# Performance work log

Hardware: AMD Instinct MI355X
Metric: run time of the kernel (lower is better)

The kernel has to match this reference:

```python
import jax, jax.numpy as jnp
import numpy as np

C = 256
HEADS = 4
RADIUS = 2
LN_EPS = 1e-5


def setup_inputs() -> dict:
    key = jax.random.key(0)
    ks = jax.random.split(key, 8)
    s = 0.02
    return {
        "feat": jax.random.normal(ks[0], (8, C, 64, 64), dtype=jnp.float32),
        "in_w": jax.random.normal(ks[1], (3 * C, C), dtype=jnp.float32) * s,
        "in_b": jnp.zeros((3 * C,), dtype=jnp.float32),
        "out_w": jax.random.normal(ks[2], (C, C), dtype=jnp.float32) * s,
        "out_b": jnp.zeros((C,), dtype=jnp.float32),
        "proj_w": jax.random.normal(ks[3], (C, 4 * C), dtype=jnp.float32) * s,
        "proj_b": jnp.zeros((C,), dtype=jnp.float32),
        "ln_g": jnp.ones((C,), dtype=jnp.float32),
        "ln_b": jnp.zeros((C,), dtype=jnp.float32),
    }


def _spatial_mask(h, w, radius):
    yy, xx = jnp.meshgrid(jnp.arange(h), jnp.arange(w), indexing="ij")
    coords = jnp.stack([yy.ravel(), xx.ravel()], axis=-1).astype(jnp.float32)  # [N,2]
    dist = jnp.abs(coords[:, None, :] - coords[None, :, :]).sum(-1)  # Manhattan [N,N]
    return jnp.where(dist > radius, -jnp.inf, 0.0).astype(jnp.float32)


def _attend(qf, mf, mask, in_w, in_b, out_w, out_b, proj_w, proj_b, ln_g, ln_b):
    b, c, h, w = qf.shape
    n = h * w
    d = c // HEADS
    qt = qf.reshape(b, c, n).transpose(0, 2, 1)  # [B,N,C]
    mt = mf.reshape(b, c, n).transpose(0, 2, 1)
    q = qt @ in_w[:c].T + in_b[:c]
    k = mt @ in_w[c:2 * c].T + in_b[c:2 * c]
    v = mt @ in_w[2 * c:].T + in_b[2 * c:]
    # [B,H,N,D]
    q = q.reshape(b, n, HEADS, d).transpose(0, 2, 1, 3)
    k = k.reshape(b, n, HEADS, d).transpose(0, 2, 1, 3)
    v = v.reshape(b, n, HEADS, d).transpose(0, 2, 1, 3)
    scores = jnp.einsum("bhnd,bhmd->bhnm", q, k) / jnp.sqrt(jnp.float32(d)) + mask
    attn = jax.nn.softmax(scores, axis=-1)
    ctx = jnp.einsum("bhnm,bhmd->bhnd", attn, v)
    ctx = ctx.transpose(0, 2, 1, 3).reshape(b, n, c) @ out_w.T + out_b  # [B,N,C]
    asym = jnp.concatenate([qt, ctx, jnp.abs(qt - ctx), qt * ctx], axis=-1)
    y = asym @ proj_w.T + proj_b
    mu = y.mean(-1, keepdims=True)
    var = ((y - mu) ** 2).mean(-1, keepdims=True)
    y = (y - mu) / jnp.sqrt(var + LN_EPS) * ln_g + ln_b
    y = jax.nn.relu(y)
    return y.transpose(0, 2, 1).reshape(b, c, h, w)


def reference(feat, in_w, in_b, out_w, out_b, proj_w, proj_b, ln_g, ln_b):
    b, c, h, w = feat.shape
    mid = w // 2
    left = feat[:, :, :, :mid]
    right = feat[:, :, :, mid:]
    right_mirror = right[:, :, :, ::-1]
    left_mirror = left[:, :, :, ::-1]
    mask = _spatial_mask(h, mid, RADIUS)
    args = (mask, in_w, in_b, out_w, out_b, proj_w, proj_b, ln_g, ln_b)
    left_asym = _attend(left, right_mirror, *args)
    right_asym = _attend(right, left_mirror, *args)
    return jnp.concatenate([left_asym, right_asym], axis=-1)
```

## Files before the change

### kernel.cpp

```cpp
#include <hip/hip_runtime.h>
#include <hip/hip_bf16.h>


#define NTOK 32768

using bf16x8 = __attribute__((ext_vector_type(8))) short;
using f32x4  = __attribute__((ext_vector_type(4))) float;

__device__ __forceinline__ float b2f(short s) {
    unsigned u = ((unsigned)(unsigned short)s) << 16;
    union { unsigned u; float f; } c; c.u = u; return c.f;
}
__device__ __forceinline__ short f2b(float f) {
    __hip_bfloat16 h = __float2bfloat16(f);
    return *(short*)&h;
}
__device__ __forceinline__ void async_copy16(const void* g, void* l) {
    __builtin_amdgcn_global_load_lds(
        (const __attribute__((address_space(1))) unsigned int*)g,
        (__attribute__((address_space(3))) unsigned int*)l, 16, 0, 0);
}

__global__ __launch_bounds__(256) void prep_kernel(const float* __restrict__ feat,
                                                   const float* __restrict__ in_w,
                                                   const float* __restrict__ out_w,
                                                   const float* __restrict__ proj_w,
                                                   __hip_bfloat16* __restrict__ X,
                                                   __hip_bfloat16* __restrict__ wbf) {
    const int bid = blockIdx.x;
    const int tid = threadIdx.x;
    if (bid < 4096) {
        __shared__ float tile[32][68];
        const int b   = bid >> 9;
        const int rem = bid & 511;
        const int sp0 = (rem & 63) * 64;
        const int c0  = (rem >> 6) * 32;
        #pragma unroll
        for (int u = 0; u < 2; ++u) {
            const int idx = tid + u * 256;
            const int cl = idx >> 4;
            const int sq = (idx & 15) * 4;
            const float4 v = *(const float4*)(feat + ((size_t)(b * 256 + c0 + cl) << 12) + sp0 + sq);
            tile[cl][sq]     = v.x;
            tile[cl][sq + 1] = v.y;
            tile[cl][sq + 2] = v.z;
            tile[cl][sq + 3] = v.w;
        }
        __syncthreads();
        #pragma unroll
        for (int u = 0; u < 2; ++u) {
            const int idx = tid + u * 256;
            const int tok = idx >> 3;
            const int cq  = (idx & 7) * 4;
            short4 s;
            s.x = f2b(tile[cq][tok]);
            s.y = f2b(tile[cq + 1][tok]);
            s.z = f2b(tile[cq + 2][tok]);
            s.w = f2b(tile[cq + 3][tok]);
            *(short4*)(X + (size_t)(b * 4096 + sp0 + tok) * 256 + c0 + cq) = s;
        }
    } else {
        const int i4 = (bid - 4096) * 1024 + tid * 4;
        if (i4 < 196608) {
            const float4 v = *(const float4*)(in_w + i4);
            short4 s = {f2b(v.x), f2b(v.y), f2b(v.z), f2b(v.w)};
            *(short4*)(wbf + i4) = s;
        }
        if (i4 < 65536) {
            const float4 v = *(const float4*)(out_w + i4);
            short4 s = {f2b(v.x), f2b(v.y), f2b(v.z), f2b(v.w)};
            *(short4*)(wbf + 196608 + i4) = s;
        }
        if (i4 < 262144) {
            const float4 v = *(const float4*)(proj_w + i4);
            short4 s = {f2b(v.x), f2b(v.y), f2b(v.z), f2b(v.w)};
            *(short4*)(wbf + 262144 + i4) = s;
        }
    }
}

template <int KDIM, bool OUT_BF16>
__global__ __launch_bounds__(256) void mfma_gemm(const __hip_bfloat16* __restrict__ A,
                                                 const __hip_bfloat16* __restrict__ W,
                                                 const float* __restrict__ bias,
                                                 void* __restrict__ C, int Ntot) {
    __shared__ __align__(16) short As[128 * 64];
    __shared__ __align__(16) short Bs[128 * 64];
    const int tid = threadIdx.x;
    const int m0 = blockIdx.x * 128;
    const int n0 = blockIdx.y * 128;
    const int wave = tid >> 6, lane = tid & 63;
    const int wm = (wave >> 1) * 64;
    const int wn = (wave & 1) * 64;
    const int fm = lane & 15;
    const int fq = lane >> 4;

    f32x4 acc[4][4] = {};

    for (int k0 = 0; k0 < KDIM; k0 += 64) {
        #pragma unroll
        for (int v = 0; v < 4; ++v) {
            const int qb = v * 256 + wave * 64;
            const int q = qb + lane;
            const int r = q >> 3;
            const int cs = (q & 7) ^ (r & 7);
            async_copy16(A + (size_t)(m0 + r) * KDIM + k0 + cs * 8, &As[qb * 8]);
            async_copy16(W + (size_t)(n0 + r) * KDIM + k0 + cs * 8, &Bs[qb * 8]);
        }
        __syncthreads();
        #pragma unroll
        for (int kk = 0; kk < 2; ++kk) {
            bf16x8 af[4], bw[4];
            #pragma unroll
            for (int i = 0; i < 4; ++i) {
                const int row = wm + i * 16 + fm;
                af[i] = *(const bf16x8*)(&As[row * 64 + (((fq + kk * 4) ^ (fm & 7)) * 8)]);
            }
            #pragma unroll
            for (int j = 0; j < 4; ++j) {
                const int row = wn + j * 16 + fm;
                bw[j] = *(const bf16x8*)(&Bs[row * 64 + (((fq + kk * 4) ^ (fm & 7)) * 8)]);
            }
            #pragma unroll
            for (int i = 0; i < 4; ++i)
                #pragma unroll
                for (int j = 0; j < 4; ++j)
                    acc[i][j] = __builtin_amdgcn_mfma_f32_16x16x32_bf16(af[i], bw[j], acc[i][j], 0, 0, 0);
        }
        __syncthreads();
    }
    #pragma unroll
    for (int j = 0; j < 4; ++j) {
        const int col = n0 + wn + j * 16 + fm;
        const float bv = bias[col];
        #pragma unroll
        for (int i = 0; i < 4; ++i) {
            #pragma unroll
            for (int r = 0; r < 4; ++r) {
                const int row = m0 + wm + i * 16 + fq * 4 + r;
                const float v = acc[i][j][r] + bv;
                if (OUT_BF16)
                    ((__hip_bfloat16*)C)[(size_t)row * Ntot + col] = __float2bfloat16(v);
                else
                    ((float*)C)[(size_t)row * Ntot + col] = v;
            }
        }
    }
}

#define P0DY ((2u)|(2u<<3)|(2u<<6)|(2u<<9)|(2u<<12)|(1u<<15)|(1u<<18)|(1u<<21))
#define P0DX ((2u)|(1u<<3)|(3u<<6)|(0u<<9)|(4u<<12)|(2u<<15)|(1u<<18)|(3u<<21))
#define P1DY ((3u)|(3u<<3)|(3u<<6)|(0u<<9)|(4u<<12)|(2u<<15)|(2u<<18)|(2u<<21))
#define P1DX ((2u)|(1u<<3)|(3u<<6)|(2u<<9)|(2u<<12)|(2u<<15)|(2u<<18)|(2u<<21))

__global__ __launch_bounds__(256) void attn_kernel(const __hip_bfloat16* __restrict__ qkv,
                                                   __hip_bfloat16* __restrict__ ctx) {
    const int t = blockIdx.x * 4 + (threadIdx.x >> 6);
    const int lane = threadIdx.x & 63;
    const int n  = lane >> 3;
    const int cg = lane & 7;
    const int x6 = t & 63;
    const int yq = (t >> 6) & 63;
    const int b  = t >> 12;
    const int side = x6 >> 5;
    const int x = x6 & 31;

    bool valid[2];
    size_t kb[2];
    #pragma unroll
    for (int p = 0; p < 2; ++p) {
        const unsigned dyp = p ? P1DY : P0DY;
        const unsigned dxp = p ? P1DX : P0DX;
        const int sh = 3 * n;
        const int dy = (int)((dyp >> sh) & 7) - 2;
        const int dx = (int)((dxp >> sh) & 7) - 2;
        const int yy = yq + dy, xx = x + dx;
        valid[p] = (p == 0 || n < 5) && yy >= 0 && yy < 64 && xx >= 0 && xx < 32;
        const int xm = side ? (31 - xx) : (63 - xx);
        int tm = (b << 12) + (yy << 6) + xm;
        if (!valid[p]) tm = t;
        kb[p] = (size_t)tm * 768 + 256 + cg * 8;
    }
    const size_t qb = (size_t)t * 768 + cg * 8;
    const size_t ob = (size_t)t * 256;

    #pragma unroll
    for (int hp = 0; hp < 2; ++hp) {
        bf16x8 q8[2], k8[2][2], v8[2][2];
        #pragma unroll
        for (int hh = 0; hh < 2; ++hh) {
            const int h = hp * 2 + hh;
            q8[hh] = *(const bf16x8*)(qkv + qb + h * 64);
            #pragma unroll
            for (int p = 0; p < 2; ++p) {
                k8[hh][p] = *(const bf16x8*)(qkv + kb[p] + h * 64);
                v8[hh][p] = *(const bf16x8*)(qkv + kb[p] + h * 64 + 256);
            }
        }
        #pragma unroll
        for (int hh = 0; hh < 2; ++hh) {
            float sc[2];
            #pragma unroll
            for (int p = 0; p < 2; ++p) {
                float s = 0.f;
                #pragma unroll
                for (int j = 0; j < 8; ++j) s += b2f(q8[hh][j]) * b2f(k8[hh][p][j]);
                s += __shfl_xor(s, 1, 64);
                s += __shfl_xor(s, 2, 64);
                s += __shfl_xor(s, 4, 64);
                sc[p] = valid[p] ? s * 0.125f : -1e30f;
            }
            const float p0 = __expf(sc[0]);
            const float p1 = __expf(sc[1]);
            float l = p0 + p1;
            l += __shfl_xor(l, 8, 64);
            l += __shfl_xor(l, 16, 64);
            l += __shfl_xor(l, 32, 64);

            float o[8];
            #pragma unroll
            for (int j = 0; j < 8; ++j)
                o[j] = p0 * b2f(v8[hh][0][j]) + p1 * b2f(v8[hh][1][j]);
            float r4[4];
            #pragma unroll
            for (int i = 0; i < 4; ++i) {
                const float a = o[2 * i], bb = o[2 * i + 1];
                const float mine = (n & 1) ? bb : a;
                const float theirs = (n & 1) ? a : bb;
                r4[i] = mine + __shfl_xor(theirs, 8, 64);
            }
            float r2[2];
            #pragma unroll
            for (int i = 0; i < 2; ++i) {
                const float a = r4[2 * i], bb = r4[2 * i + 1];
                const float mine = (n & 2) ? bb : a;
                const float theirs = (n & 2) ? a : bb;
                r2[i] = mine + __shfl_xor(theirs, 16, 64);
            }
            float ov;
            {
                const float a = r2[0], bb = r2[1];
                const float mine = (n & 4) ? bb : a;
                const float theirs = (n & 4) ? a : bb;
                ov = mine + __shfl_xor(theirs, 32, 64);
            }
            const float rl = __builtin_amdgcn_rcpf(l);
            ctx[ob + (hp * 2 + hh) * 64 + cg * 8 + n] = __float2bfloat16(ov * rl);
        }
    }
}

__global__ __launch_bounds__(512, 4) void proj_ln_fused(const __hip_bfloat16* __restrict__ X,
                                                        const __hip_bfloat16* __restrict__ CTX,
                                                        const __hip_bfloat16* __restrict__ W2,
                                                        const float* __restrict__ out_b,
                                                        const __hip_bfloat16* __restrict__ W,
                                                        const float* __restrict__ bias,
                                                        const float* __restrict__ ln_g,
                                                        const float* __restrict__ ln_b,
                                                        float* __restrict__ out) {
    __shared__ __align__(16) short smem[36864];
    __shared__ float mu_s[64], inv_s[64];
    short* c2s = smem;
    short* As  = smem + 16384;
    short* Bs  = smem + 20480;
    const int tid = threadIdx.x;
    const int m0 = blockIdx.x * 64;
    const int b = m0 >> 12, sp0 = m0 & 4095;
    const int wave = tid >> 6, lane = tid & 63;
    const int wmh = (wave >> 2) * 32;
    const int wn  = (wave & 3) * 64;
    const int fm = lane & 15;
    const int fq = lane >> 4;

    {
        f32x4 acc2[2][4] = {};
        for (int k0 = 0; k0 < 256; k0 += 64) {
            {
                const int q = tid;
                const int r = q >> 3;
                const int cs = (q & 7) ^ (r & 7);
                async_copy16(CTX + (size_t)(m0 + r) * 256 + k0 + cs * 8, &As[(wave * 64) * 8]);
            }
            #pragma unroll
            for (int v = 0; v < 4; ++v) {
                const int q = v * 512 + tid;
                const int r = q >> 3;
                const int cs = (q & 7) ^ (r & 7);
                async_copy16(W2 + (size_t)r * 256 + k0 + cs * 8, &Bs[(v * 512 + wave * 64) * 8]);
            }
            __syncthreads();
            #pragma unroll
            for (int kk = 0; kk < 2; ++kk) {
                bf16x8 af[2], bw[4];
                #pragma unroll
                for (int i = 0; i < 2; ++i) {
                    const int row = wmh + i * 16 + fm;
                    af[i] = *(const bf16x8*)(&As[row * 64 + (((fq + kk * 4) ^ (fm & 7)) * 8)]);
                }
                #pragma unroll
                for (int j = 0; j < 4; ++j) {
                    const int row = wn + j * 16 + fm;
                    bw[j] = *(const bf16x8*)(&Bs[row * 64 + (((fq + kk * 4) ^ (fm & 7)) * 8)]);
                }
                #pragma unroll
                for (int i = 0; i < 2; ++i)
                    #pragma unroll
                    for (int j = 0; j < 4; ++j)
                        acc2[i][j] = __builtin_amdgcn_mfma_f32_16x16x32_bf16(af[i], bw[j], acc2[i][j], 0, 0, 0);
            }
            __syncthreads();
        }
        #pragma unroll
        for (int j = 0; j < 4; ++j) {
            const int col = wn + j * 16 + fm;
            const float bv = out_b[col];
            const int jch = col >> 3, cl = col & 7;
            #pragma unroll
            for (int i = 0; i < 2; ++i)
                #pragma unroll
                for (int rr = 0; rr < 4; ++rr) {
                    const int row = wmh + i * 16 + fq * 4 + rr;
                    const int slot = (jch & 24) | ((jch & 7) ^ (row & 7));
                    c2s[row * 256 + slot * 8 + cl] = f2b(acc2[i][j][rr] + bv);
                }
        }
    }
    __syncthreads();

    f32x4 acc[2][4] = {};
    for (int k0 = 0; k0 < 1024; k0 += 64) {
        const int g = k0 >> 8;
        const int cb = k0 & 255;
        #pragma unroll
        for (int v = 0; v < 4; ++v) {
            const int q = v * 512 + tid;
            const int r = q >> 3;
            const int cs = (q & 7) ^ (r & 7);
            async_copy16(W + (size_t)r * 1024 + k0 + cs * 8, &Bs[(v * 512 + wave * 64) * 8]);
        }
        if (g == 0) {
            const int q = tid;
            const int r = q >> 3;
            const int cs = (q & 7) ^ (r & 7);
            async_copy16(X + (size_t)(m0 + r) * 256 + cb + cs * 8, &As[(wave * 64) * 8]);
        } else if (g >= 2) {
            const int q = tid;
            const int r = q >> 3;
            const int cs = (q & 7) ^ (r & 7);
            int4 qraw = *(const int4*)(X + (size_t)(m0 + r) * 256 + cb + cs * 8);
            const int jch = (cb >> 3) + cs;
            const int slot = (jch & 24) | ((jch & 7) ^ (r & 7));
            int4 craw = *(const int4*)(&c2s[r * 256 + slot * 8]);
            const short* qs = (const short*)&qraw;
            const short* cw = (const short*)&craw;
            short tmp[8];
            #pragma unroll
            for (int j = 0; j < 8; ++j) {
                const float qv = b2f(qs[j]), cv = b2f(cw[j]);
                tmp[j] = f2b(g == 2 ? fabsf(qv - cv) : qv * cv);
            }
            *(int4*)(&As[q * 8]) = *(int4*)tmp;
        }
        __syncthreads();
        #pragma unroll
        for (int kk = 0; kk < 2; ++kk) {
            bf16x8 af[2], bw[4];
            if (g == 1) {
                #pragma unroll
                for (int i = 0; i < 2; ++i) {
                    const int row = wmh + i * 16 + fm;
                    const int jch = (cb >> 3) + fq + kk * 4;
                    const int slot = (jch & 24) | ((jch & 7) ^ (row & 7));
                    af[i] = *(const bf16x8*)(&c2s[row * 256 + slot * 8]);
                }
            } else {
                #pragma unroll
                for (int i = 0; i < 2; ++i) {
                    const int row = wmh + i * 16 + fm;
                    af[i] = *(const bf16x8*)(&As[row * 64 + (((fq + kk * 4) ^ (fm & 7)) * 8)]);
                }
            }
            #pragma unroll
            for (int j = 0; j < 4; ++j) {
                const int row = wn + j * 16 + fm;
                bw[j] = *(const bf16x8*)(&Bs[row * 64 + (((fq + kk * 4) ^ (fm & 7)) * 8)]);
            }
            #pragma unroll
            for (int i = 0; i < 2; ++i)
                #pragma unroll
                for (int j = 0; j < 4; ++j)
                    acc[i][j] = __builtin_amdgcn_mfma_f32_16x16x32_bf16(af[i], bw[j], acc[i][j], 0, 0, 0);
        }
        __syncthreads();
    }
    short* ys = smem;
    #pragma unroll
    for (int j = 0; j < 4; ++j) {
        const int col = wn + j * 16 + fm;
        const float bv = bias[col];
        #pragma unroll
        for (int i = 0; i < 2; ++i)
            #pragma unroll
            for (int r = 0; r < 4; ++r)
                ys[(wmh + i * 16 + fq * 4 + r) * 266 + col] = f2b(acc[i][j][r] + bv);
    }
    __syncthreads();
    {
        const int tt = tid >> 3, seg = tid & 7;
        float s = 0.f, ss = 0.f;
        #pragma unroll
        for (int j = 0; j < 32; ++j) {
            const float v = b2f(ys[tt * 266 + seg * 32 + j]);
            s += v; ss += v * v;
        }
        s += __shfl_xor(s, 1, 64);  ss += __shfl_xor(ss, 1, 64);
        s += __shfl_xor(s, 2, 64);  ss += __shfl_xor(ss, 2, 64);
        s += __shfl_xor(s, 4, 64);  ss += __shfl_xor(ss, 4, 64);
        if (seg == 0) {
            const float mu = s * (1.f / 256.f);
            const float var = ss * (1.f / 256.f) - mu * mu;
            mu_s[tt] = mu;
            inv_s[tt] = rsqrtf(var + 1e-5f);
        }
    }
    __syncthreads();
    {
        const int tl = tid & 63;
        const int j0 = tid >> 6;
        const float mu = mu_s[tl], inv = inv_s[tl];
        #pragma unroll
        for (int u = 0; u < 32; ++u) {
            const int j = j0 * 32 + u;
            const float v = (b2f(ys[tl * 266 + j]) - mu) * inv * ln_g[j] + ln_b[j];
            out[((size_t)(b * 256 + j) << 12) + sp0 + tl] = fmaxf(v, 0.f);
        }
    }
}

extern "C" void kernel_launch(void* const* d_in, const int* in_sizes, int n_in,
                              void* d_out, int out_size, void* d_ws, size_t ws_size,
                              hipStream_t stream) {
    (void)in_sizes; (void)n_in; (void)out_size; (void)ws_size;
    const float* feat   = (const float*)d_in[0];
    const float* in_w   = (const float*)d_in[1];
    const float* in_b   = (const float*)d_in[2];
    const float* out_w  = (const float*)d_in[3];
    const float* out_b  = (const float*)d_in[4];
    const float* proj_w = (const float*)d_in[5];
    const float* proj_b = (const float*)d_in[6];
    const float* ln_g   = (const float*)d_in[7];
    const float* ln_b   = (const float*)d_in[8];
    float* out = (float*)d_out;

    char* ws = (char*)d_ws;
    __hip_bfloat16* Xbf  = (__hip_bfloat16*)(ws);
    __hip_bfloat16* wbf  = (__hip_bfloat16*)(ws + (size_t)(16) * (1 << 20));
    __hip_bfloat16* qkv  = (__hip_bfloat16*)(ws + (size_t)(17) * (1 << 20));
    __hip_bfloat16* ctx  = (__hip_bfloat16*)(ws + (size_t)(65) * (1 << 20));
    __hip_bfloat16* in_wbf   = wbf;
    __hip_bfloat16* out_wbf  = wbf + 196608;
    __hip_bfloat16* proj_wbf = wbf + 262144;

    prep_kernel   <<<4352, 256, 0, stream>>>(feat, in_w, out_w, proj_w, Xbf, wbf);
    mfma_gemm<256, true><<<dim3(256, 6), 256, 0, stream>>>(Xbf, in_wbf, in_b, qkv, 768);
    attn_kernel   <<<NTOK / 4, 256, 0, stream>>>(qkv, ctx);
    proj_ln_fused <<<NTOK / 64, 512, 0, stream>>>(Xbf, ctx, out_wbf, out_b,
                                                  proj_wbf, proj_b, ln_g, ln_b, out);
}
```

Baseline: 184.8 us.

## Load weight fragments directly from global and stage full activation rows in LDS

The generic GEMM and the fused projection+LayerNorm kernel now read weight fragments straight from global memory (through cache) into registers instead of staging them in LDS. The activation tile for the full K extent is loaded once up front, and the per-k-step barriers are dropped. The projection loop is restructured to compute |q-ctx| and q*ctx chunks together and to read X directly from global. This removes LDS traffic and synchronization but relies on L2/L1 for weight reuse, uses uncoalesced per-lane global loads, and enlarges LDS use in the GEMM (64KB), which may reduce occupancy.

```diff
diff --git a/kernel.cpp b/kernel.cpp
--- a/kernel.cpp
+++ b/kernel.cpp
@@ -84,8 +84,7 @@
                                                  const __hip_bfloat16* __restrict__ W,
                                                  const float* __restrict__ bias,
                                                  void* __restrict__ C, int Ntot) {
-    __shared__ __align__(16) short As[128 * 64];
-    __shared__ __align__(16) short Bs[128 * 64];
+    __shared__ __align__(16) short As[128 * 256];
     const int tid = threadIdx.x;
     const int m0 = blockIdx.x * 128;
     const int n0 = blockIdx.y * 128;
@@ -95,31 +94,33 @@
     const int fm = lane & 15;
     const int fq = lane >> 4;
 
+    #pragma unroll
+    for (int v = 0; v < 16; ++v) {
+        const int q = v * 256 + tid;
+        const int r = q >> 5;
+        const int sl = q & 31;
+        const int gc = (sl & 24) | ((sl & 7) ^ (r & 7));
+        async_copy16(A + (size_t)(m0 + r) * KDIM + gc * 8, &As[(v * 256 + wave * 64) * 8]);
+    }
+    __syncthreads();
+
     f32x4 acc[4][4] = {};
-
+    #pragma unroll
     for (int k0 = 0; k0 < KDIM; k0 += 64) {
         #pragma unroll
-        for (int v = 0; v < 4; ++v) {
-            const int qb = v * 256 + wave * 64;
-            const int q = qb + lane;
-            const int r = q >> 3;
-            const int cs = (q & 7) ^ (r & 7);
-            async_copy16(A + (size_t)(m0 + r) * KDIM + k0 + cs * 8, &As[qb * 8]);
-            async_copy16(W + (size_t)(n0 + r) * KDIM + k0 + cs * 8, &Bs[qb * 8]);
-        }
-        __syncthreads();
-        #pragma unroll
         for (int kk = 0; kk < 2; ++kk) {
+            const int jj = (k0 >> 3) + fq + kk * 4;
             bf16x8 af[4], bw[4];
             #pragma unroll
             for (int i = 0; i < 4; ++i) {
                 const int row = wm + i * 16 + fm;
-                af[i] = *(const bf16x8*)(&As[row * 64 + (((fq + kk * 4) ^ (fm & 7)) * 8)]);
+                const int sl = (jj & 24) | ((jj & 7) ^ (row & 7));
+                af[i] = *(const bf16x8*)(&As[row * 256 + sl * 8]);
             }
             #pragma unroll
             for (int j = 0; j < 4; ++j) {
-                const int row = wn + j * 16 + fm;
-                bw[j] = *(const bf16x8*)(&Bs[row * 64 + (((fq + kk * 4) ^ (fm & 7)) * 8)]);
+                const int row = n0 + wn + j * 16 + fm;
+                bw[j] = *(const bf16x8*)(W + (size_t)row * KDIM + k0 + (fq + kk * 4) * 8);
             }
             #pragma unroll
             for (int i = 0; i < 4; ++i)
@@ -127,7 +128,6 @@
                 for (int j = 0; j < 4; ++j)
                     acc[i][j] = __builtin_amdgcn_mfma_f32_16x16x32_bf16(af[i], bw[j], acc[i][j], 0, 0, 0);
         }
-        __syncthreads();
     }
     #pragma unroll
     for (int j = 0; j < 4; ++j) {
@@ -261,9 +261,10 @@
                                                         float* __restrict__ out) {
     __shared__ __align__(16) short smem[36864];
     __shared__ float mu_s[64], inv_s[64];
-    short* c2s = smem;
-    short* As  = smem + 16384;
-    short* Bs  = smem + 20480;
+    short* ctx_s = smem;
+    short* c2s   = smem + 16384;
+    short* As2   = smem;
+    short* As3   = smem + 4096;
     const int tid = threadIdx.x;
     const int m0 = blockIdx.x * 64;
     const int b = m0 >> 12, sp0 = m0 & 4095;
@@ -273,35 +274,34 @@
     const int fm = lane & 15;
     const int fq = lane >> 4;
 
+    #pragma unroll
+    for (int v = 0; v < 4; ++v) {
+        const int q = v * 512 + tid;
+        const int r = q >> 5;
+        const int sl = q & 31;
+        const int gc = (sl & 24) | ((sl & 7) ^ (r & 7));
+        async_copy16(CTX + (size_t)(m0 + r) * 256 + gc * 8, &ctx_s[(v * 512 + wave * 64) * 8]);
+    }
+    __syncthreads();
+
     {
         f32x4 acc2[2][4] = {};
+        #pragma unroll
         for (int k0 = 0; k0 < 256; k0 += 64) {
-            {
-                const int q = tid;
-                const int r = q >> 3;
-                const int cs = (q & 7) ^ (r & 7);
-                async_copy16(CTX + (size_t)(m0 + r) * 256 + k0 + cs * 8, &As[(wave * 64) * 8]);
-            }
-            #pragma unroll
-            for (int v = 0; v < 4; ++v) {
-                const int q = v * 512 + tid;
-                const int r = q >> 3;
-                const int cs = (q & 7) ^ (r & 7);
-                async_copy16(W2 + (size_t)r * 256 + k0 + cs * 8, &Bs[(v * 512 + wave * 64) * 8]);
-            }
-            __syncthreads();
             #pragma unroll
             for (int kk = 0; kk < 2; ++kk) {
+                const int jj = (k0 >> 3) + fq + kk * 4;
                 bf16x8 af[2], bw[4];
                 #pragma unroll
                 for (int i = 0; i < 2; ++i) {
                     const int row = wmh + i * 16 + fm;
-                    af[i] = *(const bf16x8*)(&As[row * 64 + (((fq + kk * 4) ^ (fm & 7)) * 8)]);
+                    const int sl = (jj & 24) | ((jj & 7) ^ (row & 7));
+                    af[i] = *(const bf16x8*)(&ctx_s[row * 256 + sl * 8]);
                 }
                 #pragma unroll
                 for (int j = 0; j < 4; ++j) {
                     const int row = wn + j * 16 + fm;
-                    bw[j] = *(const bf16x8*)(&Bs[row * 64 + (((fq + kk * 4) ^ (fm & 7)) * 8)]);
+                    bw[j] = *(const bf16x8*)(W2 + (size_t)row * 256 + k0 + (fq + kk * 4) * 8);
                 }
                 #pragma unroll
                 for (int i = 0; i < 2; ++i)
@@ -309,7 +309,6 @@
                     for (int j = 0; j < 4; ++j)
                         acc2[i][j] = __builtin_amdgcn_mfma_f32_16x16x32_bf16(af[i], bw[j], acc2[i][j], 0, 0, 0);
             }
-            __syncthreads();
         }
         #pragma unroll
         for (int j = 0; j < 4; ++j) {
@@ -329,71 +328,63 @@
     __syncthreads();
 
     f32x4 acc[2][4] = {};
-    for (int k0 = 0; k0 < 1024; k0 += 64) {
-        const int g = k0 >> 8;
-        const int cb = k0 & 255;
-        #pragma unroll
-        for (int v = 0; v < 4; ++v) {
-            const int q = v * 512 + tid;
-            const int r = q >> 3;
-            const int cs = (q & 7) ^ (r & 7);
-            async_copy16(W + (size_t)r * 1024 + k0 + cs * 8, &Bs[(v * 512 + wave * 64) * 8]);
-        }
-        if (g == 0) {
-            const int q = tid;
-            const int r = q >> 3;
-            const int cs = (q & 7) ^ (r & 7);
-            async_copy16(X + (size_t)(m0 + r) * 256 + cb + cs * 8, &As[(wave * 64) * 8]);
-        } else if (g >= 2) {
-            const int q = tid;
-            const int r = q >> 3;
-            const int cs = (q & 7) ^ (r & 7);
-            int4 qraw = *(const int4*)(X + (size_t)(m0 + r) * 256 + cb + cs * 8);
-            const int jch = (cb >> 3) + cs;
-            const int slot = (jch & 24) | ((jch & 7) ^ (r & 7));
-            int4 craw = *(const int4*)(&c2s[r * 256 + slot * 8]);
+    for (int cbs = 0; cbs < 4; ++cbs) {
+        const int cb = cbs * 64;
+        const int cr = tid >> 3;
+        const int cs = (tid & 7) ^ (cr & 7);
+        int4 qraw = *(const int4*)(X + (size_t)(m0 + cr) * 256 + cb + cs * 8);
+        const int cjch = (cb >> 3) + cs;
+        const int cslot = (cjch & 24) | ((cjch & 7) ^ (cr & 7));
+        int4 craw = *(const int4*)(&c2s[cr * 256 + cslot * 8]);
+        __syncthreads();
+        {
             const short* qs = (const short*)&qraw;
             const short* cw = (const short*)&craw;
-            short tmp[8];
+            short t2[8], t3[8];
             #pragma unroll
             for (int j = 0; j < 8; ++j) {
                 const float qv = b2f(qs[j]), cv = b2f(cw[j]);
-                tmp[j] = f2b(g == 2 ? fabsf(qv - cv) : qv * cv);
-            }
-            *(int4*)(&As[q * 8]) = *(int4*)tmp;
+                t2[j] = f2b(fabsf(qv - cv));
+                t3[j] = f2b(qv * cv);
+            }
+            *(int4*)(&As2[tid * 8]) = *(int4*)t2;
+            *(int4*)(&As3[tid * 8]) = *(int4*)t3;
         }
         __syncthreads();
         #pragma unroll
-        for (int kk = 0; kk < 2; ++kk) {
-            bf16x8 af[2], bw[4];
-            if (g == 1) {
+        for (int g = 0; g < 4; ++g) {
+            #pragma unroll
+            for (int kk = 0; kk < 2; ++kk) {
+                bf16x8 af[2], bw[4];
+                #pragma unroll
+                for (int j = 0; j < 4; ++j) {
+                    const int row = wn + j * 16 + fm;
+                    bw[j] = *(const bf16x8*)(W + (size_t)row * 1024 + g * 256 + cb + (fq + kk * 4) * 8);
+                }
                 #pragma unroll
                 for (int i = 0; i < 2; ++i) {
                     const int row = wmh + i * 16 + fm;
-                    const int jch = (cb >> 3) + fq + kk * 4;
-                    const int slot = (jch & 24) | ((jch & 7) ^ (row & 7));
-                    af[i] = *(const bf16x8*)(&c2s[row * 256 + slot * 8]);
+                    if (g == 0) {
+                        af[i] = *(const bf16x8*)(X + (size_t)(m0 + row) * 256 + cb + (fq + kk * 4) * 8);
+                    } else if (g == 1) {
+                        const int jj = (cb >> 3) + fq + kk * 4;
+                        const int sl = (jj & 24) | ((jj & 7) ^ (row & 7));
+                        af[i] = *(const bf16x8*)(&c2s[row * 256 + sl * 8]);
+                    } else {
+                        const short* Ag = (g == 2) ? As2 : As3;
+                        af[i] = *(const bf16x8*)(&Ag[row * 64 + (((fq + kk * 4) ^ (row & 7)) * 8)]);
+                    }
                 }
-            } else {
-                #pragma unroll
-                for (int i = 0; i < 2; ++i) {
-                    const int row = wmh + i * 16 + fm;
-                    af[i] = *(const bf16x8*)(&As[row * 64 + (((fq + kk * 4) ^ (fm & 7)) * 8)]);
-                }
-            }
-            #pragma unroll
-            for (int j = 0; j < 4; ++j) {
-                const int row = wn + j * 16 + fm;
-                bw[j] = *(const bf16x8*)(&Bs[row * 64 + (((fq + kk * 4) ^ (fm & 7)) * 8)]);
-            }
-            #pragma unroll
-            for (int i = 0; i < 2; ++i)
-                #pragma unroll
-                for (int j = 0; j < 4; ++j)
-                    acc[i][j] = __builtin_amdgcn_mfma_f32_16x16x32_bf16(af[i], bw[j], acc[i][j], 0, 0, 0);
-        }
-        __syncthreads();
-    }
+                #pragma unroll
+                for (int i = 0; i < 2; ++i)
+                    #pragma unroll
+                    for (int j = 0; j < 4; ++j)
+                        acc[i][j] = __builtin_amdgcn_mfma_f32_16x16x32_bf16(af[i], bw[j], acc[i][j], 0, 0, 0);
+            }
+        }
+    }
+    __syncthreads();
+
     short* ys = smem;
     #pragma unroll
     for (int j = 0; j < 4; ++j) {
```

Result: slower. 250.3 us (+35.5%).

## Double-buffer LDS tiles in QKV GEMM and fused proj/LN kernel

Applied to the files above, without the earlier changes.

Both the generic MFMA GEMM and the fused out-proj/proj/LayerNorm kernel now use ping-pong LDS buffers, so the next K-tile's weight loads are issued before computing on the current one. This removes one barrier per iteration and hides global-load latency. In the fused kernel the full CTX and X row tiles are preloaded into LDS once, and the |q-c| and q*c features are built in registers from those LDS copies. The kernel's LDS use grows to 128KB and the launch-bounds occupancy hint drops from 4 to 2 blocks, so fewer blocks can be resident.

```diff
diff --git a/kernel.cpp b/kernel.cpp
--- a/kernel.cpp
+++ b/kernel.cpp
@@ -84,8 +84,8 @@
                                                  const __hip_bfloat16* __restrict__ W,
                                                  const float* __restrict__ bias,
                                                  void* __restrict__ C, int Ntot) {
-    __shared__ __align__(16) short As[128 * 64];
-    __shared__ __align__(16) short Bs[128 * 64];
+    __shared__ __align__(16) short As[2][128 * 64];
+    __shared__ __align__(16) short Bs[2][128 * 64];
     const int tid = threadIdx.x;
     const int m0 = blockIdx.x * 128;
     const int n0 = blockIdx.y * 128;
@@ -95,31 +95,44 @@
     const int fm = lane & 15;
     const int fq = lane >> 4;
 
+    #pragma unroll
+    for (int v = 0; v < 4; ++v) {
+        const int qb = v * 256 + wave * 64;
+        const int q = qb + lane;
+        const int r = q >> 3;
+        const int cs = (q & 7) ^ (r & 7);
+        async_copy16(A + (size_t)(m0 + r) * KDIM + cs * 8, &As[0][qb * 8]);
+        async_copy16(W + (size_t)(n0 + r) * KDIM + cs * 8, &Bs[0][qb * 8]);
+    }
+    __syncthreads();
+
     f32x4 acc[4][4] = {};
-
-    for (int k0 = 0; k0 < KDIM; k0 += 64) {
-        #pragma unroll
-        for (int v = 0; v < 4; ++v) {
-            const int qb = v * 256 + wave * 64;
-            const int q = qb + lane;
-            const int r = q >> 3;
-            const int cs = (q & 7) ^ (r & 7);
-            async_copy16(A + (size_t)(m0 + r) * KDIM + k0 + cs * 8, &As[qb * 8]);
-            async_copy16(W + (size_t)(n0 + r) * KDIM + k0 + cs * 8, &Bs[qb * 8]);
-        }
-        __syncthreads();
+    #pragma unroll
+    for (int t = 0; t < KDIM / 64; ++t) {
+        const int cur = t & 1;
+        if (t + 1 < KDIM / 64) {
+            #pragma unroll
+            for (int v = 0; v < 4; ++v) {
+                const int qb = v * 256 + wave * 64;
+                const int q = qb + lane;
+                const int r = q >> 3;
+                const int cs = (q & 7) ^ (r & 7);
+                async_copy16(A + (size_t)(m0 + r) * KDIM + (t + 1) * 64 + cs * 8, &As[cur ^ 1][qb * 8]);
+                async_copy16(W + (size_t)(n0 + r) * KDIM + (t + 1) * 64 + cs * 8, &Bs[cur ^ 1][qb * 8]);
+            }
+        }
         #pragma unroll
         for (int kk = 0; kk < 2; ++kk) {
             bf16x8 af[4], bw[4];
             #pragma unroll
             for (int i = 0; i < 4; ++i) {
                 const int row = wm + i * 16 + fm;
-                af[i] = *(const bf16x8*)(&As[row * 64 + (((fq + kk * 4) ^ (fm & 7)) * 8)]);
+                af[i] = *(const bf16x8*)(&As[cur][row * 64 + (((fq + kk * 4) ^ (fm & 7)) * 8)]);
             }
             #pragma unroll
             for (int j = 0; j < 4; ++j) {
                 const int row = wn + j * 16 + fm;
-                bw[j] = *(const bf16x8*)(&Bs[row * 64 + (((fq + kk * 4) ^ (fm & 7)) * 8)]);
+                bw[j] = *(const bf16x8*)(&Bs[cur][row * 64 + (((fq + kk * 4) ^ (fm & 7)) * 8)]);
             }
             #pragma unroll
             for (int i = 0; i < 4; ++i)
@@ -250,7 +263,7 @@
     }
 }
 
-__global__ __launch_bounds__(512, 4) void proj_ln_fused(const __hip_bfloat16* __restrict__ X,
+__global__ __launch_bounds__(512, 2) void proj_ln_fused(const __hip_bfloat16* __restrict__ X,
                                                         const __hip_bfloat16* __restrict__ CTX,
                                                         const __hip_bfloat16* __restrict__ W2,
                                                         const float* __restrict__ out_b,
@@ -259,11 +272,12 @@
                                                         const float* __restrict__ ln_g,
                                                         const float* __restrict__ ln_b,
                                                         float* __restrict__ out) {
-    __shared__ __align__(16) short smem[36864];
+    __shared__ __align__(16) short smem[65536];
     __shared__ float mu_s[64], inv_s[64];
-    short* c2s = smem;
-    short* As  = smem + 16384;
-    short* Bs  = smem + 20480;
+    short* S0  = smem;
+    short* c2s = smem + 16384;
+    short* Bs0 = smem + 32768;
+    short* Bs1 = smem + 49152;
     const int tid = threadIdx.x;
     const int m0 = blockIdx.x * 64;
     const int b = m0 >> 12, sp0 = m0 & 4095;
@@ -273,118 +287,135 @@
     const int fm = lane & 15;
     const int fq = lane >> 4;
 
-    {
-        f32x4 acc2[2][4] = {};
-        for (int k0 = 0; k0 < 256; k0 += 64) {
-            {
-                const int q = tid;
-                const int r = q >> 3;
-                const int cs = (q & 7) ^ (r & 7);
-                async_copy16(CTX + (size_t)(m0 + r) * 256 + k0 + cs * 8, &As[(wave * 64) * 8]);
-            }
+    #pragma unroll
+    for (int v = 0; v < 4; ++v) {
+        const int q = v * 512 + tid;
+        const int r = q >> 5;
+        const int sl = q & 31;
+        const int gc = (sl & 24) | ((sl & 7) ^ (r & 7));
+        async_copy16(CTX + (size_t)(m0 + r) * 256 + gc * 8, &S0[(v * 512 + wave * 64) * 8]);
+    }
+    #pragma unroll
+    for (int v = 0; v < 4; ++v) {
+        const int q = v * 512 + tid;
+        const int r = q >> 3;
+        const int cs = (q & 7) ^ (r & 7);
+        async_copy16(W2 + (size_t)r * 256 + cs * 8, &Bs0[(v * 512 + wave * 64) * 8]);
+    }
+    __syncthreads();
+
+    f32x4 acc2[2][4] = {};
+    #pragma unroll
+    for (int t = 0; t < 4; ++t) {
+        short* bsc = (t & 1) ? Bs1 : Bs0;
+        short* bsn = (t & 1) ? Bs0 : Bs1;
+        if (t < 3) {
             #pragma unroll
             for (int v = 0; v < 4; ++v) {
                 const int q = v * 512 + tid;
                 const int r = q >> 3;
                 const int cs = (q & 7) ^ (r & 7);
-                async_copy16(W2 + (size_t)r * 256 + k0 + cs * 8, &Bs[(v * 512 + wave * 64) * 8]);
-            }
-            __syncthreads();
-            #pragma unroll
-            for (int kk = 0; kk < 2; ++kk) {
-                bf16x8 af[2], bw[4];
-                #pragma unroll
-                for (int i = 0; i < 2; ++i) {
-                    const int row = wmh + i * 16 + fm;
-                    af[i] = *(const bf16x8*)(&As[row * 64 + (((fq + kk * 4) ^ (fm & 7)) * 8)]);
-                }
-                #pragma unroll
-                for (int j = 0; j < 4; ++j) {
-                    const int row = wn + j * 16 + fm;
-                    bw[j] = *(const bf16x8*)(&Bs[row * 64 + (((fq + kk * 4) ^ (fm & 7)) * 8)]);
-                }
-                #pragma unroll
-                for (int i = 0; i < 2; ++i)
-                    #pragma unroll
-                    for (int j = 0; j < 4; ++j)
-                        acc2[i][j] = __builtin_amdgcn_mfma_f32_16x16x32_bf16(af[i], bw[j], acc2[i][j], 0, 0, 0);
-            }
-            __syncthreads();
-        }
-        #pragma unroll
-        for (int j = 0; j < 4; ++j) {
-            const int col = wn + j * 16 + fm;
-            const float bv = out_b[col];
-            const int jch = col >> 3, cl = col & 7;
+                async_copy16(W2 + (size_t)r * 256 + (t + 1) * 64 + cs * 8, &bsn[(v * 512 + wave * 64) * 8]);
+            }
+        }
+        #pragma unroll
+        for (int kk = 0; kk < 2; ++kk) {
+            const int jj = t * 8 + fq + kk * 4;
+            bf16x8 af[2], bw[4];
+            #pragma unroll
+            for (int i = 0; i < 2; ++i) {
+                const int row = wmh + i * 16 + fm;
+                const int sl = (jj & 24) | ((jj & 7) ^ (row & 7));
+                af[i] = *(const bf16x8*)(&S0[row * 256 + sl * 8]);
+            }
+            #pragma unroll
+            for (int j = 0; j < 4; ++j) {
+                const int row = wn + j * 16 + fm;
+                bw[j] = *(const bf16x8*)(&bsc[row * 64 + (((fq + kk * 4) ^ (fm & 7)) * 8)]);
+            }
             #pragma unroll
             for (int i = 0; i < 2; ++i)
                 #pragma unroll
-                for (int rr = 0; rr < 4; ++rr) {
-                    const int row = wmh + i * 16 + fq * 4 + rr;
-                    const int slot = (jch & 24) | ((jch & 7) ^ (row & 7));
-                    c2s[row * 256 + slot * 8 + cl] = f2b(acc2[i][j][rr] + bv);
-                }
-        }
+                for (int j = 0; j < 4; ++j)
+                    acc2[i][j] = __builtin_amdgcn_mfma_f32_16x16x32_bf16(af[i], bw[j], acc2[i][j], 0, 0, 0);
+        }
+        __syncthreads();
+    }
+
+    #pragma unroll
+    for (int j = 0; j < 4; ++j) {
+        const int col = wn + j * 16 + fm;
+        const float bv = out_b[col];
+        const int jch = col >> 3, cl = col & 7;
+        #pragma unroll
+        for (int i = 0; i < 2; ++i)
+            #pragma unroll
+            for (int rr = 0; rr < 4; ++rr) {
+                const int row = wmh + i * 16 + fq * 4 + rr;
+                const int slot = (jch & 24) | ((jch & 7) ^ (row & 7));
+                c2s[row * 256 + slot * 8 + cl] = f2b(acc2[i][j][rr] + bv);
+            }
+    }
+    #pragma unroll
+    for (int v = 0; v < 4; ++v) {
+        const int q = v * 512 + tid;
+        const int r = q >> 5;
+        const int sl = q & 31;
+        const int gc = (sl & 24) | ((sl & 7) ^ (r & 7));
+        async_copy16(X + (size_t)(m0 + r) * 256 + gc * 8, &S0[(v * 512 + wave * 64) * 8]);
+    }
+    #pragma unroll
+    for (int v = 0; v < 4; ++v) {
+        const int q = v * 512 + tid;
+        const int r = q >> 3;
+        const int cs = (q & 7) ^ (r & 7);
+        async_copy16(W + (size_t)r * 1024 + cs * 8, &Bs0[(v * 512 + wave * 64) * 8]);
     }
     __syncthreads();
 
     f32x4 acc[2][4] = {};
-    for (int k0 = 0; k0 < 1024; k0 += 64) {
-        const int g = k0 >> 8;
-        const int cb = k0 & 255;
-        #pragma unroll
-        for (int v = 0; v < 4; ++v) {
-            const int q = v * 512 + tid;
-            const int r = q >> 3;
-            const int cs = (q & 7) ^ (r & 7);
-            async_copy16(W + (size_t)r * 1024 + k0 + cs * 8, &Bs[(v * 512 + wave * 64) * 8]);
-        }
-        if (g == 0) {
-            const int q = tid;
-            const int r = q >> 3;
-            const int cs = (q & 7) ^ (r & 7);
-            async_copy16(X + (size_t)(m0 + r) * 256 + cb + cs * 8, &As[(wave * 64) * 8]);
-        } else if (g >= 2) {
-            const int q = tid;
-            const int r = q >> 3;
-            const int cs = (q & 7) ^ (r & 7);
-            int4 qraw = *(const int4*)(X + (size_t)(m0 + r) * 256 + cb + cs * 8);
-            const int jch = (cb >> 3) + cs;
-            const int slot = (jch & 24) | ((jch & 7) ^ (r & 7));
-            int4 craw = *(const int4*)(&c2s[r * 256 + slot * 8]);
-            const short* qs = (const short*)&qraw;
-            const short* cw = (const short*)&craw;
-            short tmp[8];
-            #pragma unroll
-            for (int j = 0; j < 8; ++j) {
-                const float qv = b2f(qs[j]), cv = b2f(cw[j]);
-                tmp[j] = f2b(g == 2 ? fabsf(qv - cv) : qv * cv);
-            }
-            *(int4*)(&As[q * 8]) = *(int4*)tmp;
-        }
-        __syncthreads();
+    #pragma unroll
+    for (int t = 0; t < 16; ++t) {
+        short* bsc = (t & 1) ? Bs1 : Bs0;
+        short* bsn = (t & 1) ? Bs0 : Bs1;
+        if (t < 15) {
+            #pragma unroll
+            for (int v = 0; v < 4; ++v) {
+                const int q = v * 512 + tid;
+                const int r = q >> 3;
+                const int cs = (q & 7) ^ (r & 7);
+                async_copy16(W + (size_t)r * 1024 + (t + 1) * 64 + cs * 8, &bsn[(v * 512 + wave * 64) * 8]);
+            }
+        }
+        const int g = t >> 2;
         #pragma unroll
         for (int kk = 0; kk < 2; ++kk) {
+            const int jj = (t & 3) * 8 + fq + kk * 4;
             bf16x8 af[2], bw[4];
-            if (g == 1) {
-                #pragma unroll
-                for (int i = 0; i < 2; ++i) {
-                    const int row = wmh + i * 16 + fm;
-                    const int jch = (cb >> 3) + fq + kk * 4;
-                    const int slot = (jch & 24) | ((jch & 7) ^ (row & 7));
-                    af[i] = *(const bf16x8*)(&c2s[row * 256 + slot * 8]);
-                }
-            } else {
-                #pragma unroll
-                for (int i = 0; i < 2; ++i) {
-                    const int row = wmh + i * 16 + fm;
-                    af[i] = *(const bf16x8*)(&As[row * 64 + (((fq + kk * 4) ^ (fm & 7)) * 8)]);
+            #pragma unroll
+            for (int i = 0; i < 2; ++i) {
+                const int row = wmh + i * 16 + fm;
+                const int sl = (jj & 24) | ((jj & 7) ^ (row & 7));
+                if (g == 0) {
+                    af[i] = *(const bf16x8*)(&S0[row * 256 + sl * 8]);
+                } else if (g == 1) {
+                    af[i] = *(const bf16x8*)(&c2s[row * 256 + sl * 8]);
+                } else {
+                    const bf16x8 qe = *(const bf16x8*)(&S0[row * 256 + sl * 8]);
+                    const bf16x8 ce = *(const bf16x8*)(&c2s[row * 256 + sl * 8]);
+                    bf16x8 rr;
+                    #pragma unroll
+                    for (int e = 0; e < 8; ++e) {
+                        const float a = b2f(qe[e]), c = b2f(ce[e]);
+                        rr[e] = f2b(g == 2 ? fabsf(a - c) : a * c);
+                    }
+                    af[i] = rr;
                 }
             }
             #pragma unroll
             for (int j = 0; j < 4; ++j) {
                 const int row = wn + j * 16 + fm;
-                bw[j] = *(const bf16x8*)(&Bs[row * 64 + (((fq + kk * 4) ^ (fm & 7)) * 8)]);
+                bw[j] = *(const bf16x8*)(&bsc[row * 64 + (((fq + kk * 4) ^ (fm & 7)) * 8)]);
             }
             #pragma unroll
             for (int i = 0; i < 2; ++i)
@@ -394,6 +425,7 @@
         }
         __syncthreads();
     }
+
     short* ys = smem;
     #pragma unroll
     for (int j = 0; j < 4; ++j) {
```

Result: slower. 201.2 us (+8.9%).

## Double-buffer QKV GEMM LDS tiles and remap blocks for XCD locality

Applied to the files above, without the earlier changes.

The QKV projection GEMM now keeps two LDS buffers for its A and W tiles. It prefetches the next K-slice with async global-to-LDS copies while the current slice feeds the MFMA instructions, so load latency can hide behind compute. The 2D grid becomes a 1D grid with a swizzled block-to-tile mapping, so neighbouring tiles run on the same XCD and can share L2. The cost is double the LDS per block, which may lower occupancy, and the K loop has only four iterations, so there is little latency to hide.

```diff
diff --git a/kernel.cpp b/kernel.cpp
--- a/kernel.cpp
+++ b/kernel.cpp
@@ -84,42 +84,56 @@
                                                  const __hip_bfloat16* __restrict__ W,
                                                  const float* __restrict__ bias,
                                                  void* __restrict__ C, int Ntot) {
-    __shared__ __align__(16) short As[128 * 64];
-    __shared__ __align__(16) short Bs[128 * 64];
+    __shared__ __align__(16) short As[2][128 * 64];
+    __shared__ __align__(16) short Bs[2][128 * 64];
     const int tid = threadIdx.x;
-    const int m0 = blockIdx.x * 128;
-    const int n0 = blockIdx.y * 128;
+    const int work = (blockIdx.x & 7) * 192 + (blockIdx.x >> 3);
+    const int m0 = (work / 6) * 128;
+    const int n0 = (work % 6) * 128;
     const int wave = tid >> 6, lane = tid & 63;
     const int wm = (wave >> 1) * 64;
     const int wn = (wave & 1) * 64;
     const int fm = lane & 15;
     const int fq = lane >> 4;
 
+    #pragma unroll
+    for (int v = 0; v < 4; ++v) {
+        const int qb = v * 256 + wave * 64;
+        const int q = qb + lane;
+        const int r = q >> 3;
+        const int cs = (q & 7) ^ (r & 7);
+        async_copy16(A + (size_t)(m0 + r) * KDIM + cs * 8, &As[0][qb * 8]);
+        async_copy16(W + (size_t)(n0 + r) * KDIM + cs * 8, &Bs[0][qb * 8]);
+    }
+    __syncthreads();
+
     f32x4 acc[4][4] = {};
-
-    for (int k0 = 0; k0 < KDIM; k0 += 64) {
-        #pragma unroll
-        for (int v = 0; v < 4; ++v) {
-            const int qb = v * 256 + wave * 64;
-            const int q = qb + lane;
-            const int r = q >> 3;
-            const int cs = (q & 7) ^ (r & 7);
-            async_copy16(A + (size_t)(m0 + r) * KDIM + k0 + cs * 8, &As[qb * 8]);
-            async_copy16(W + (size_t)(n0 + r) * KDIM + k0 + cs * 8, &Bs[qb * 8]);
-        }
-        __syncthreads();
+    #pragma unroll
+    for (int t = 0; t < KDIM / 64; ++t) {
+        const int cur = t & 1;
+        if (t + 1 < KDIM / 64) {
+            #pragma unroll
+            for (int v = 0; v < 4; ++v) {
+                const int qb = v * 256 + wave * 64;
+                const int q = qb + lane;
+                const int r = q >> 3;
+                const int cs = (q & 7) ^ (r & 7);
+                async_copy16(A + (size_t)(m0 + r) * KDIM + (t + 1) * 64 + cs * 8, &As[cur ^ 1][qb * 8]);
+                async_copy16(W + (size_t)(n0 + r) * KDIM + (t + 1) * 64 + cs * 8, &Bs[cur ^ 1][qb * 8]);
+            }
+        }
         #pragma unroll
         for (int kk = 0; kk < 2; ++kk) {
             bf16x8 af[4], bw[4];
             #pragma unroll
             for (int i = 0; i < 4; ++i) {
                 const int row = wm + i * 16 + fm;
-                af[i] = *(const bf16x8*)(&As[row * 64 + (((fq + kk * 4) ^ (fm & 7)) * 8)]);
+                af[i] = *(const bf16x8*)(&As[cur][row * 64 + (((fq + kk * 4) ^ (fm & 7)) * 8)]);
             }
             #pragma unroll
             for (int j = 0; j < 4; ++j) {
                 const int row = wn + j * 16 + fm;
-                bw[j] = *(const bf16x8*)(&Bs[row * 64 + (((fq + kk * 4) ^ (fm & 7)) * 8)]);
+                bw[j] = *(const bf16x8*)(&Bs[cur][row * 64 + (((fq + kk * 4) ^ (fm & 7)) * 8)]);
             }
             #pragma unroll
             for (int i = 0; i < 4; ++i)
@@ -463,7 +477,7 @@
     __hip_bfloat16* proj_wbf = wbf + 262144;
 
     prep_kernel   <<<4352, 256, 0, stream>>>(feat, in_w, out_w, proj_w, Xbf, wbf);
-    mfma_gemm<256, true><<<dim3(256, 6), 256, 0, stream>>>(Xbf, in_wbf, in_b, qkv, 768);
+    mfma_gemm<256, true><<<1536, 256, 0, stream>>>(Xbf, in_wbf, in_b, qkv, 768);
     attn_kernel   <<<NTOK / 4, 256, 0, stream>>>(qkv, ctx);
     proj_ln_fused <<<NTOK / 64, 512, 0, stream>>>(Xbf, ctx, out_wbf, out_b,
                                                   proj_wbf, proj_b, ln_g, ln_b, out);
```

Result: faster. 180.8 us (-2.1%).
